# Kernel optimization log

Measured on AMD Instinct MI355X. Metric: run time of the kernel, lower is better.

Reference implementation:

```python
import jax, jax.numpy as jnp
import numpy as np

B, N, D = 4096, 64, 128

def setup_inputs() -> dict:
    key = jax.random.key(0)
    ks = jax.random.split(key, 5)
    return {
        "stu_emb": jax.random.normal(ks[0], (B, D), jnp.float32),
        "concept_emb": jax.random.normal(ks[1], (B, D), jnp.float32),
        "neighbor_emb": jax.random.normal(ks[2], (B, N, D), jnp.float32),
        # Linear(2D -> D) for stu_concept_integration (xavier-like scale)
        "Ws": jax.random.normal(ks[3], (2 * D, D), jnp.float32) * (2.0 / (3 * D)) ** 0.5,
        "bs": jnp.full((D,), 0.1, jnp.float32),
        # Linear(2D -> 1) for concept_neighbor_weight
        "Ww": jax.random.normal(ks[4], (2 * D, 1), jnp.float32) * (2.0 / (2 * D + 1)) ** 0.5,
        "bw": jnp.full((1,), 0.1, jnp.float32),
    }


def reference(stu_emb, concept_emb, neighbor_emb, Ws, bs, Ww, bw):
    # Masks: 1 where the (first) concatenated input is nonzero along features
    dt = stu_emb.dtype
    mask_s = (jnp.sum(stu_emb, -1, keepdims=True) != 0).astype(dt)[:, None, :]      # [B,1,1]
    mask_c = (jnp.sum(concept_emb, -1, keepdims=True) != 0).astype(dt)[:, None, :]  # [B,1,1]

    # Split concat-linear into two halves so the broadcasted half is computed once
    Ws_a, Ws_b = Ws[:D], Ws[D:]   # [D,D] each
    Ww_a, Ww_b = Ww[:D], Ww[D:]   # [D,1] each

    stu_part = stu_emb @ Ws_a            # [B,D]
    con_part = concept_emb @ Ws_b        # [B,D]
    nbr_part = neighbor_emb @ Ws_b       # [B,N,D]

    # neighbor attention weights: Linear(2D->1)(cat(concept_ext, neighbor)) * mask_c
    w = (concept_emb @ Ww_a)[:, None, :] + neighbor_emb @ Ww_b + bw  # [B,N,1]
    w = w * mask_c
    w = jax.nn.softmax(w, axis=-2)  # softmax over neighbor axis

    # stu integrated with neighbors / with the original concept, masked by stu mask
    integ_n = (stu_part[:, None, :] + nbr_part + bs) * mask_s            # [B,N,D]
    integ_o = (stu_part[:, None, :] + con_part[:, None, :] + bs) * mask_s  # [B,N,D] (broadcast)

    # combine over neighbor axis and average the two branches
    y = jnp.sum(integ_o + w * integ_n, axis=-2) / 2  # [B,D]
    return y
```

## Files before the change

### kernel.cpp

```cpp
#include <hip/hip_runtime.h>

#define BB 4096
#define NN 64
#define DD 128
#define G  4

__global__ __launch_bounds__(256) void kFused(
    const float* __restrict__ stu,
    const float* __restrict__ conc,
    const float* __restrict__ nbr,
    const float* __restrict__ Ws,
    const float* __restrict__ bs,
    const float* __restrict__ Ww,
    float* __restrict__ y)
{
    const int t  = threadIdx.x;
    const int b0 = blockIdx.x * G;

    __shared__ float logits[NN];
    __shared__ float wsm[NN];
    __shared__ float sred[2][2];
    __shared__ float maskh[G];
    __shared__ __align__(16) float u[G][2 * DD];
    __shared__ __align__(16) float scratch[8 * G * DD];

    const int cg = t & 31;
    const int g8 = t >> 5;
    const float4 wb = reinterpret_cast<const float4*>(Ww + DD)[cg];

    for (int g = 0; g < G; ++g) {
        const int b = b0 + g;
        const float4* nb4 = reinterpret_cast<const float4*>(nbr + (size_t)b * NN * DD);

        float4 val[8];
#pragma unroll
        for (int i = 0; i < 8; ++i) val[i] = nb4[t + 256 * i];

#pragma unroll
        for (int i = 0; i < 8; ++i) {
            float x = val[i].x * wb.x + val[i].y * wb.y + val[i].z * wb.z + val[i].w * wb.w;
            x += __shfl_xor(x, 1);
            x += __shfl_xor(x, 2);
            x += __shfl_xor(x, 4);
            x += __shfl_xor(x, 8);
            x += __shfl_xor(x, 16);
            if (cg == 0) logits[g8 + 8 * i] = x;
        }

        if (t < DD) {
            float cs = conc[(size_t)b * DD + t];
            float ss = stu [(size_t)b * DD + t];
            u[g][t]      = 65.0f * ss;
            u[g][DD + t] = 64.0f * cs;
            float c2 = cs, s2 = ss;
            c2 += __shfl_xor(c2, 1);  s2 += __shfl_xor(s2, 1);
            c2 += __shfl_xor(c2, 2);  s2 += __shfl_xor(s2, 2);
            c2 += __shfl_xor(c2, 4);  s2 += __shfl_xor(s2, 4);
            c2 += __shfl_xor(c2, 8);  s2 += __shfl_xor(s2, 8);
            c2 += __shfl_xor(c2, 16); s2 += __shfl_xor(s2, 16);
            c2 += __shfl_xor(c2, 32); s2 += __shfl_xor(s2, 32);
            if ((t & 63) == 0) { sred[t >> 6][0] = c2; sred[t >> 6][1] = s2; }
        }
        __syncthreads();

        if (t < NN) {
            float csum = sred[0][0] + sred[1][0];
            float l = logits[t];
            float m = l;
            m = fmaxf(m, __shfl_xor(m, 1));
            m = fmaxf(m, __shfl_xor(m, 2));
            m = fmaxf(m, __shfl_xor(m, 4));
            m = fmaxf(m, __shfl_xor(m, 8));
            m = fmaxf(m, __shfl_xor(m, 16));
            m = fmaxf(m, __shfl_xor(m, 32));
            float e = __expf(l - m);
            float s = e;
            s += __shfl_xor(s, 1);
            s += __shfl_xor(s, 2);
            s += __shfl_xor(s, 4);
            s += __shfl_xor(s, 8);
            s += __shfl_xor(s, 16);
            s += __shfl_xor(s, 32);
            wsm[t] = (csum != 0.0f) ? (e / s) : (1.0f / 64.0f);
        }
        if (t == 0) maskh[g] = ((sred[0][1] + sred[1][1]) != 0.0f) ? 0.5f : 0.0f;
        __syncthreads();

        float4 a = {0.f, 0.f, 0.f, 0.f};
#pragma unroll
        for (int i = 0; i < 8; ++i) {
            float w = wsm[g8 + 8 * i];
            a.x += w * val[i].x; a.y += w * val[i].y;
            a.z += w * val[i].z; a.w += w * val[i].w;
        }
        reinterpret_cast<float4*>(scratch)[g8 * 32 + cg] = a;
        __syncthreads();

        if (t < DD) {
            float s = 0.0f;
#pragma unroll
            for (int k = 0; k < 8; ++k) s += scratch[k * DD + t];
            u[g][DD + t] += s;
        }
        __syncthreads();
    }

    const int kg = t >> 5;
    float4 acc0 = {0,0,0,0}, acc1 = {0,0,0,0}, acc2 = {0,0,0,0}, acc3 = {0,0,0,0};
    const float4* Ws4 = reinterpret_cast<const float4*>(Ws);
#pragma unroll 4
    for (int j = 0; j < 32; ++j) {
        const int k = kg * 32 + j;
        float4 wv = Ws4[k * 32 + cg];
        float u0 = u[0][k], u1 = u[1][k], u2 = u[2][k], u3 = u[3][k];
        acc0.x += u0 * wv.x; acc0.y += u0 * wv.y; acc0.z += u0 * wv.z; acc0.w += u0 * wv.w;
        acc1.x += u1 * wv.x; acc1.y += u1 * wv.y; acc1.z += u1 * wv.z; acc1.w += u1 * wv.w;
        acc2.x += u2 * wv.x; acc2.y += u2 * wv.y; acc2.z += u2 * wv.z; acc2.w += u2 * wv.w;
        acc3.x += u3 * wv.x; acc3.y += u3 * wv.y; acc3.z += u3 * wv.z; acc3.w += u3 * wv.w;
    }
    {
        float4* pr = reinterpret_cast<float4*>(scratch);
        pr[(kg * G + 0) * 32 + cg] = acc0;
        pr[(kg * G + 1) * 32 + cg] = acc1;
        pr[(kg * G + 2) * 32 + cg] = acc2;
        pr[(kg * G + 3) * 32 + cg] = acc3;
    }
    __syncthreads();
#pragma unroll
    for (int i = 0; i < 2; ++i) {
        const int idx = t + 256 * i;
        const int r = idx >> 7;
        const int c = idx & 127;
        float s = 0.0f;
#pragma unroll
        for (int k2 = 0; k2 < 8; ++k2) s += scratch[(k2 * G + r) * DD + c];
        y[(size_t)(b0 + r) * DD + c] = (s + 65.0f * bs[c]) * maskh[r];
    }
}

extern "C" void kernel_launch(void* const* d_in, const int* in_sizes, int n_in,
                              void* d_out, int out_size, void* d_ws, size_t ws_size,
                              hipStream_t stream) {
    const float* stu  = (const float*)d_in[0];
    const float* conc = (const float*)d_in[1];
    const float* nbr  = (const float*)d_in[2];
    const float* Ws   = (const float*)d_in[3];
    const float* bs   = (const float*)d_in[4];
    const float* Ww   = (const float*)d_in[5];
    float* y = (float*)d_out;

    kFused<<<BB / G, 256, 0, stream>>>(stu, conc, nbr, Ws, bs, Ww, y);
}
```

Before: 33.07 us.

## Prefetch next row's neighbors and compute softmax redundantly per wave to cut barriers

Register double-buffers the neighbor tile so the next batch row's loads are in flight while the current row is processed. Every wave now recomputes the mask sums and the softmax itself and broadcasts weights with shuffles, replacing shared-memory handoffs and removing two of the four barriers per row. It also reduces the weighted neighbor sum within each wave before writing to shared memory, and adds a launch-bounds occupancy hint. In exchange it doubles the neighbor registers per thread, which may reduce occupancy or cause spills, and repeats the stu/concept loads and softmax in every wave.

```diff
diff --git a/kernel.cpp b/kernel.cpp
--- a/kernel.cpp
+++ b/kernel.cpp
@@ -5,7 +5,7 @@
 #define DD 128
 #define G  4
 
-__global__ __launch_bounds__(256) void kFused(
+__global__ __launch_bounds__(256, 4) void kFused(
     const float* __restrict__ stu,
     const float* __restrict__ conc,
     const float* __restrict__ nbr,
@@ -14,31 +14,64 @@
     const float* __restrict__ Ww,
     float* __restrict__ y)
 {
-    const int t  = threadIdx.x;
-    const int b0 = blockIdx.x * G;
+    const int t    = threadIdx.x;
+    const int lane = t & 63;
+    const int cg   = t & 31;
+    const int g8   = t >> 5;
+    const int wv   = t >> 6;
+    const int b0   = blockIdx.x * G;
 
     __shared__ float logits[NN];
-    __shared__ float wsm[NN];
-    __shared__ float sred[2][2];
-    __shared__ float maskh[G];
     __shared__ __align__(16) float u[G][2 * DD];
+    __shared__ __align__(16) float part[4 * DD];
     __shared__ __align__(16) float scratch[8 * G * DD];
 
-    const int cg = t & 31;
-    const int g8 = t >> 5;
     const float4 wb = reinterpret_cast<const float4*>(Ww + DD)[cg];
 
+    float msk0 = 0.f, msk1 = 0.f, msk2 = 0.f, msk3 = 0.f;
+
+    const float4* nb4 = reinterpret_cast<const float4*>(nbr);
+    float4 val[8], valn[8];
+#pragma unroll
+    for (int i = 0; i < 8; ++i) val[i] = nb4[(size_t)b0 * 2048 + t + 256 * i];
+
+#pragma unroll
     for (int g = 0; g < G; ++g) {
         const int b = b0 + g;
-        const float4* nb4 = reinterpret_cast<const float4*>(nbr + (size_t)b * NN * DD);
 
-        float4 val[8];
+        if (g < G - 1) {
 #pragma unroll
-        for (int i = 0; i < 8; ++i) val[i] = nb4[t + 256 * i];
+            for (int i = 0; i < 8; ++i)
+                valn[i] = nb4[(size_t)(b + 1) * 2048 + t + 256 * i];
+        }
+
+        float cv0 = conc[(size_t)b * DD + lane];
+        float cv1 = conc[(size_t)b * DD + 64 + lane];
+        float sv0 = stu [(size_t)b * DD + lane];
+        float sv1 = stu [(size_t)b * DD + 64 + lane];
+        float cs = cv0 + cv1, ss = sv0 + sv1;
+#pragma unroll
+        for (int o = 1; o < 64; o <<= 1) {
+            cs += __shfl_xor(cs, o);
+            ss += __shfl_xor(ss, o);
+        }
+        const float mg = (ss != 0.0f) ? 0.5f : 0.0f;
+        if      (g == 0) msk0 = mg;
+        else if (g == 1) msk1 = mg;
+        else if (g == 2) msk2 = mg;
+        else             msk3 = mg;
+
+        if (t < 64) {
+            u[g][t]           = 65.0f * sv0;
+            u[g][t + 64]      = 65.0f * sv1;
+            u[g][DD + t]      = 64.0f * cv0;
+            u[g][DD + 64 + t] = 64.0f * cv1;
+        }
 
 #pragma unroll
         for (int i = 0; i < 8; ++i) {
-            float x = val[i].x * wb.x + val[i].y * wb.y + val[i].z * wb.z + val[i].w * wb.w;
+            float x = val[i].x * wb.x + val[i].y * wb.y
+                    + val[i].z * wb.z + val[i].w * wb.w;
             x += __shfl_xor(x, 1);
             x += __shfl_xor(x, 2);
             x += __shfl_xor(x, 4);
@@ -46,96 +79,87 @@
             x += __shfl_xor(x, 16);
             if (cg == 0) logits[g8 + 8 * i] = x;
         }
-
-        if (t < DD) {
-            float cs = conc[(size_t)b * DD + t];
-            float ss = stu [(size_t)b * DD + t];
-            u[g][t]      = 65.0f * ss;
-            u[g][DD + t] = 64.0f * cs;
-            float c2 = cs, s2 = ss;
-            c2 += __shfl_xor(c2, 1);  s2 += __shfl_xor(s2, 1);
-            c2 += __shfl_xor(c2, 2);  s2 += __shfl_xor(s2, 2);
-            c2 += __shfl_xor(c2, 4);  s2 += __shfl_xor(s2, 4);
-            c2 += __shfl_xor(c2, 8);  s2 += __shfl_xor(s2, 8);
-            c2 += __shfl_xor(c2, 16); s2 += __shfl_xor(s2, 16);
-            c2 += __shfl_xor(c2, 32); s2 += __shfl_xor(s2, 32);
-            if ((t & 63) == 0) { sred[t >> 6][0] = c2; sred[t >> 6][1] = s2; }
-        }
         __syncthreads();
 
-        if (t < NN) {
-            float csum = sred[0][0] + sred[1][0];
-            float l = logits[t];
-            float m = l;
-            m = fmaxf(m, __shfl_xor(m, 1));
-            m = fmaxf(m, __shfl_xor(m, 2));
-            m = fmaxf(m, __shfl_xor(m, 4));
-            m = fmaxf(m, __shfl_xor(m, 8));
-            m = fmaxf(m, __shfl_xor(m, 16));
-            m = fmaxf(m, __shfl_xor(m, 32));
-            float e = __expf(l - m);
-            float s = e;
-            s += __shfl_xor(s, 1);
-            s += __shfl_xor(s, 2);
-            s += __shfl_xor(s, 4);
-            s += __shfl_xor(s, 8);
-            s += __shfl_xor(s, 16);
-            s += __shfl_xor(s, 32);
-            wsm[t] = (csum != 0.0f) ? (e / s) : (1.0f / 64.0f);
-        }
-        if (t == 0) maskh[g] = ((sred[0][1] + sred[1][1]) != 0.0f) ? 0.5f : 0.0f;
-        __syncthreads();
+        float l = logits[lane];
+        float m = l;
+        m = fmaxf(m, __shfl_xor(m, 1));
+        m = fmaxf(m, __shfl_xor(m, 2));
+        m = fmaxf(m, __shfl_xor(m, 4));
+        m = fmaxf(m, __shfl_xor(m, 8));
+        m = fmaxf(m, __shfl_xor(m, 16));
+        m = fmaxf(m, __shfl_xor(m, 32));
+        float e = __expf(l - m);
+        float sden = e;
+        sden += __shfl_xor(sden, 1);
+        sden += __shfl_xor(sden, 2);
+        sden += __shfl_xor(sden, 4);
+        sden += __shfl_xor(sden, 8);
+        sden += __shfl_xor(sden, 16);
+        sden += __shfl_xor(sden, 32);
+        const float wlane = (cs != 0.0f) ? (e / sden) : (1.0f / 64.0f);
 
         float4 a = {0.f, 0.f, 0.f, 0.f};
 #pragma unroll
         for (int i = 0; i < 8; ++i) {
-            float w = wsm[g8 + 8 * i];
+            float w = __shfl(wlane, g8 + 8 * i);
             a.x += w * val[i].x; a.y += w * val[i].y;
             a.z += w * val[i].z; a.w += w * val[i].w;
         }
-        reinterpret_cast<float4*>(scratch)[g8 * 32 + cg] = a;
+        a.x += __shfl_xor(a.x, 32);
+        a.y += __shfl_xor(a.y, 32);
+        a.z += __shfl_xor(a.z, 32);
+        a.w += __shfl_xor(a.w, 32);
+        if (lane < 32)
+            reinterpret_cast<float4*>(part)[wv * 32 + cg] = a;
         __syncthreads();
 
         if (t < DD) {
-            float s = 0.0f;
+            float vsum = part[t] + part[DD + t] + part[2 * DD + t] + part[3 * DD + t];
+            u[g][DD + t] += vsum;
+        }
+
+        if (g < G - 1) {
 #pragma unroll
-            for (int k = 0; k < 8; ++k) s += scratch[k * DD + t];
-            u[g][DD + t] += s;
+            for (int i = 0; i < 8; ++i) val[i] = valn[i];
         }
-        __syncthreads();
     }
+    __syncthreads();
 
-    const int kg = t >> 5;
     float4 acc0 = {0,0,0,0}, acc1 = {0,0,0,0}, acc2 = {0,0,0,0}, acc3 = {0,0,0,0};
     const float4* Ws4 = reinterpret_cast<const float4*>(Ws);
 #pragma unroll 4
     for (int j = 0; j < 32; ++j) {
-        const int k = kg * 32 + j;
-        float4 wv = Ws4[k * 32 + cg];
+        const int k = g8 * 32 + j;
+        float4 wvv = Ws4[k * 32 + cg];
         float u0 = u[0][k], u1 = u[1][k], u2 = u[2][k], u3 = u[3][k];
-        acc0.x += u0 * wv.x; acc0.y += u0 * wv.y; acc0.z += u0 * wv.z; acc0.w += u0 * wv.w;
-        acc1.x += u1 * wv.x; acc1.y += u1 * wv.y; acc1.z += u1 * wv.z; acc1.w += u1 * wv.w;
-        acc2.x += u2 * wv.x; acc2.y += u2 * wv.y; acc2.z += u2 * wv.z; acc2.w += u2 * wv.w;
-        acc3.x += u3 * wv.x; acc3.y += u3 * wv.y; acc3.z += u3 * wv.z; acc3.w += u3 * wv.w;
+        acc0.x += u0 * wvv.x; acc0.y += u0 * wvv.y; acc0.z += u0 * wvv.z; acc0.w += u0 * wvv.w;
+        acc1.x += u1 * wvv.x; acc1.y += u1 * wvv.y; acc1.z += u1 * wvv.z; acc1.w += u1 * wvv.w;
+        acc2.x += u2 * wvv.x; acc2.y += u2 * wvv.y; acc2.z += u2 * wvv.z; acc2.w += u2 * wvv.w;
+        acc3.x += u3 * wvv.x; acc3.y += u3 * wvv.y; acc3.z += u3 * wvv.z; acc3.w += u3 * wvv.w;
     }
     {
         float4* pr = reinterpret_cast<float4*>(scratch);
-        pr[(kg * G + 0) * 32 + cg] = acc0;
-        pr[(kg * G + 1) * 32 + cg] = acc1;
-        pr[(kg * G + 2) * 32 + cg] = acc2;
-        pr[(kg * G + 3) * 32 + cg] = acc3;
+        pr[(g8 * G + 0) * 32 + cg] = acc0;
+        pr[(g8 * G + 1) * 32 + cg] = acc1;
+        pr[(g8 * G + 2) * 32 + cg] = acc2;
+        pr[(g8 * G + 3) * 32 + cg] = acc3;
     }
     __syncthreads();
+
+    const int r1 = t >> 7;
+    const int c  = t & 127;
+    const float mA = r1 ? msk1 : msk0;
+    const float mB = r1 ? msk3 : msk2;
+    float sA = 0.0f, sB = 0.0f;
 #pragma unroll
-    for (int i = 0; i < 2; ++i) {
-        const int idx = t + 256 * i;
-        const int r = idx >> 7;
-        const int c = idx & 127;
-        float s = 0.0f;
-#pragma unroll
-        for (int k2 = 0; k2 < 8; ++k2) s += scratch[(k2 * G + r) * DD + c];
-        y[(size_t)(b0 + r) * DD + c] = (s + 65.0f * bs[c]) * maskh[r];
+    for (int k2 = 0; k2 < 8; ++k2) {
+        sA += scratch[(k2 * G + r1) * DD + c];
+        sB += scratch[(k2 * G + 2 + r1) * DD + c];
     }
+    const float bc = bs[c];
+    y[(size_t)(b0 + r1) * DD + c]     = (sA + 65.0f * bc) * mA;
+    y[(size_t)(b0 + 2 + r1) * DD + c] = (sB + 65.0f * bc) * mB;
 }
 
 extern "C" void kernel_launch(void* const* d_in, const int* in_sizes, int n_in,
```

Measured after the change: 35.85 us. 1.08x slower.
